# Performance work log

Measured on AMD Instinct MI355X. Metric: run time of the kernel, lower is better.

Reference implementation:

```python
import jax, jax.numpy as jnp
import numpy as np

HEADS = 4
DIM_HEAD = 128
DIM = 128
INNER = HEADS * DIM_HEAD  # 512
MAX_POS = 100
SCALE = DIM_HEAD ** -0.5


def setup_inputs() -> dict:
    key = jax.random.key(0)
    ks = jax.random.split(key, 8)
    b, h, w = 2, 48, 64
    fmap1 = jax.random.normal(ks[0], (b, DIM, h, w), jnp.float32)
    fmap2 = jax.random.normal(ks[1], (b, DIM, h, w), jnp.float32)
    Wqk = jax.random.normal(ks[2], (2 * INNER, DIM), jnp.float32) * 0.05
    Wv = jax.random.normal(ks[3], (INNER, DIM), jnp.float32) * 0.05
    rel_h = jax.random.normal(ks[4], (2 * MAX_POS - 1, DIM_HEAD), jnp.float32) * 0.05
    rel_w = jax.random.normal(ks[5], (2 * MAX_POS - 1, DIM_HEAD), jnp.float32) * 0.05
    Wp = jax.random.normal(ks[6], (DIM, INNER), jnp.float32) * 0.05
    gamma = jnp.full((1,), 0.1, jnp.float32)  # nonzero so the attn path is active
    return {"fmap1": fmap1, "fmap2": fmap2, "Wqk": Wqk, "Wv": Wv,
            "rel_h": rel_h, "rel_w": rel_w, "Wp": Wp, "gamma": gamma}


def _aggregate(fmap, Wqk, Wv, rel_h, rel_w, Wp, gamma):
    b, c, H, W = fmap.shape
    # 1x1 conv = channel matmul
    qk = jnp.einsum('oc,bchw->bohw', Wqk, fmap)
    q = qk[:, :INNER] * SCALE  # k chunk unused (position-only similarity)
    # b (n d) h w -> b n h w d
    q = q.reshape(b, HEADS, DIM_HEAD, H, W).transpose(0, 1, 3, 4, 2)
    v = jnp.einsum('oc,bchw->bohw', Wv, fmap)
    v = v.reshape(b, HEADS, DIM_HEAD, H, W).transpose(0, 1, 3, 4, 2).reshape(b, HEADS, H * W, DIM_HEAD)
    # relative position similarity (RelPosEmb)
    idx_h = jnp.arange(H)[:, None] - jnp.arange(H)[None, :] + (MAX_POS - 1)  # (H,H)
    idx_w = jnp.arange(W)[:, None] - jnp.arange(W)[None, :] + (MAX_POS - 1)  # (W,W)
    He = rel_h[idx_h]  # (x,u,d)
    We = rel_w[idx_w]  # (y,v,d)
    hs = jnp.einsum('bnxyd,xud->bnxyu', q, He)  # (b,n,x,y,u)
    ws = jnp.einsum('bnxyd,yvd->bnxyv', q, We)  # (b,n,x,y,v)
    sim = hs[..., :, None] + ws[..., None, :]   # (b,n,x,y,u,v)
    sim = sim.reshape(b, HEADS, H * W, H * W)
    attn = jax.nn.softmax(sim, axis=-1)
    out = jnp.einsum('bnij,bnjd->bnid', attn, v)  # (b,n,hw,d)
    out = out.reshape(b, HEADS, H, W, DIM_HEAD).transpose(0, 1, 4, 2, 3).reshape(b, INNER, H, W)
    out = jnp.einsum('oc,bchw->bohw', Wp, out)  # project (dim != inner_dim)
    return fmap + gamma[0] * out


def reference(fmap1, fmap2, Wqk, Wv, rel_h, rel_w, Wp, gamma):
    out1 = _aggregate(fmap1, Wqk, Wv, rel_h, rel_w, Wp, gamma)
    out2 = _aggregate(fmap2, Wqk, Wv, rel_h, rel_w, Wp, gamma)
    return (out1, out2)
```

## Files before the change

kernel.cpp:

```cpp
#include <hip/hip_runtime.h>
#include <cstdint>
#include <cstddef>

typedef short bf16x8 __attribute__((ext_vector_type(8)));
typedef float f32x4 __attribute__((ext_vector_type(4)));

#define HH 48
#define WW 64
#define HWSZ 3072
#define SCALE_Q 0.08838834764831845f

__device__ __forceinline__ float b2f(unsigned short u) {
    union { unsigned int i; float f; } c; c.i = ((unsigned int)u) << 16; return c.f;
}
__device__ __forceinline__ unsigned short f2b(float f) {
    union { float f; unsigned int i; } c; c.f = f;
    unsigned int r = (c.i + 0x7fffu + ((c.i >> 16) & 1u)) >> 16;
    return (unsigned short)r;
}

__global__ __launch_bounds__(256) void k_transpose(const float* __restrict__ f0,
                                                   const float* __restrict__ f1,
                                                   unsigned short* __restrict__ Xb) {
    __shared__ float t[32][33];
    int fb = blockIdx.z; int f = fb >> 1, bb = fb & 1;
    const float* src = f ? f1 : f0;
    int pT = blockIdx.x * 32, cT = blockIdx.y * 32;
    int tx = threadIdx.x, ty = threadIdx.y;
#pragma unroll
    for (int i = 0; i < 4; ++i) {
        int c = cT + ty + i * 8, pos = pT + tx;
        t[ty + i * 8][tx] = src[(size_t)(bb * 128 + c) * HWSZ + pos];
    }
    __syncthreads();
#pragma unroll
    for (int i = 0; i < 4; ++i) {
        int pos = pT + ty + i * 8, c = cT + tx;
        Xb[(size_t)(fb * HWSZ + pos) * 128 + c] = f2b(t[tx][ty + i * 8]);
    }
}

__global__ __launch_bounds__(256) void k_weights(const float* __restrict__ Wqk,
                                                 const float* __restrict__ Wv,
                                                 const float* __restrict__ Wp,
                                                 unsigned short* __restrict__ Wcat,
                                                 unsigned short* __restrict__ Wpb) {
    int idx = blockIdx.x * 256 + threadIdx.x;
    if (idx < 131072) {
        int o = idx >> 7, c = idx & 127;
        float v = (o < 512) ? Wqk[o * 128 + c] * SCALE_Q : Wv[(o - 512) * 128 + c];
        Wcat[idx] = f2b(v);
    } else {
        int j = idx - 131072;
        Wpb[j] = f2b(Wp[j]);
    }
}

__global__ __launch_bounds__(256) void k_qv(const unsigned short* __restrict__ Xb,
                                            const unsigned short* __restrict__ Wcat,
                                            unsigned short* __restrict__ Qx,
                                            unsigned short* __restrict__ Vt) {
    __shared__ unsigned short Asub[64 * 136];
    __shared__ unsigned short Bsub[128 * 136];
    int mt = blockIdx.x, nt = blockIdx.y, fb = blockIdx.z;
    int tid = threadIdx.x;
    const unsigned short* asrc = Xb + (size_t)(fb * HWSZ + mt * 64) * 128;
    const unsigned short* bsrc = Wcat + (size_t)nt * 128 * 128;
    for (int ch = tid; ch < 1024; ch += 256) {
        int row = ch >> 4, seg = ch & 15;
        *(bf16x8*)&Asub[row * 136 + seg * 8] = *(const bf16x8*)(asrc + ch * 8);
    }
    for (int ch = tid; ch < 2048; ch += 256) {
        int row = ch >> 4, seg = ch & 15;
        *(bf16x8*)&Bsub[row * 136 + seg * 8] = *(const bf16x8*)(bsrc + ch * 8);
    }
    __syncthreads();
    int l = tid & 63, w = tid >> 6;
    int wm = w >> 1, wn = w & 1;
    int lr = l & 15, lk8 = (l >> 4) * 8;
    f32x4 acc[2][4] = {};
#pragma unroll
    for (int kt = 0; kt < 4; ++kt) {
        bf16x8 a[2], b[4];
#pragma unroll
        for (int m = 0; m < 2; ++m)
            a[m] = *(const bf16x8*)&Asub[(wm * 32 + m * 16 + lr) * 136 + kt * 32 + lk8];
#pragma unroll
        for (int n = 0; n < 4; ++n)
            b[n] = *(const bf16x8*)&Bsub[(wn * 64 + n * 16 + lr) * 136 + kt * 32 + lk8];
#pragma unroll
        for (int m = 0; m < 2; ++m)
#pragma unroll
            for (int n = 0; n < 4; ++n)
                acc[m][n] = __builtin_amdgcn_mfma_f32_16x16x32_bf16(a[m], b[n], acc[m][n], 0, 0, 0);
    }
    int f = fb >> 1, bb = fb & 1;
#pragma unroll
    for (int m = 0; m < 2; ++m)
#pragma unroll
        for (int n = 0; n < 4; ++n) {
            int o = nt * 128 + wn * 64 + n * 16 + lr;
            int pos0 = mt * 64 + wm * 32 + m * 16 + (l >> 4) * 4;
            if (o < 512) {
                int nh = o >> 7, d = o & 127;
#pragma unroll
                for (int r = 0; r < 4; ++r) {
                    int pos = pos0 + r, x = pos >> 6, y = pos & 63;
                    Qx[(size_t)((f * 48 + x) * 512 + (bb * 4 + nh) * 64 + y) * 128 + d] = f2b(acc[m][n][r]);
                }
            } else {
                int oo = o - 512, nh = oo >> 7, d = oo & 127;
                uint2 val;
                val.x = (unsigned int)f2b(acc[m][n][0]) | ((unsigned int)f2b(acc[m][n][1]) << 16);
                val.y = (unsigned int)f2b(acc[m][n][2]) | ((unsigned int)f2b(acc[m][n][3]) << 16);
                *(uint2*)&Vt[(size_t)((fb * 4 + nh) * 128 + d) * HWSZ + pos0] = val;
            }
        }
}

__global__ __launch_bounds__(256) void k_ph(const unsigned short* __restrict__ Qx,
                                            const float* __restrict__ rel_h,
                                            unsigned short* __restrict__ PH) {
    __shared__ float sm[4][16][52];
    int x = blockIdx.x, f = blockIdx.y, mtz = blockIdx.z;
    int tid = threadIdx.x, l = tid & 63, w = tid >> 6;
    int lr = l & 15, lk8 = (l >> 4) * 8;
    bf16x8 bh[3][4];
#pragma unroll
    for (int ut = 0; ut < 3; ++ut) {
        int u = ut * 16 + lr, rr = x - u + 99;
#pragma unroll
        for (int kt = 0; kt < 4; ++kt) {
            const float* s = rel_h + rr * 128 + kt * 32 + lk8;
            float4 a0 = *(const float4*)s, a1 = *(const float4*)(s + 4);
            bf16x8 pk;
            pk[0] = (short)f2b(a0.x); pk[1] = (short)f2b(a0.y); pk[2] = (short)f2b(a0.z); pk[3] = (short)f2b(a0.w);
            pk[4] = (short)f2b(a1.x); pk[5] = (short)f2b(a1.y); pk[6] = (short)f2b(a1.z); pk[7] = (short)f2b(a1.w);
            bh[ut][kt] = pk;
        }
    }
    const unsigned short* qbase = Qx + (size_t)(f * 48 + x) * 512 * 128;
    unsigned short* phbase = PH + (size_t)(f * 48 + x) * 512 * 48;
    for (int mt = mtz * 2; mt < mtz * 2 + 2; ++mt) {
        int rg = w * 128 + mt * 16 + lr;
        const unsigned short* qrow = qbase + (size_t)rg * 128;
        bf16x8 a[4];
#pragma unroll
        for (int kt = 0; kt < 4; ++kt) a[kt] = *(const bf16x8*)(qrow + kt * 32 + lk8);
        f32x4 acc[3] = {};
#pragma unroll
        for (int kt = 0; kt < 4; ++kt)
#pragma unroll
            for (int ut = 0; ut < 3; ++ut)
                acc[ut] = __builtin_amdgcn_mfma_f32_16x16x32_bf16(a[kt], bh[ut][kt], acc[ut], 0, 0, 0);
        __syncthreads();
#pragma unroll
        for (int ut = 0; ut < 3; ++ut)
#pragma unroll
            for (int r = 0; r < 4; ++r)
                sm[w][(l >> 4) * 4 + r][ut * 16 + lr] = acc[ut][r];
        __syncthreads();
        int part = l >> 4;
        float vb[12];
        float mx = -1e30f;
#pragma unroll
        for (int j = 0; j < 12; ++j) { vb[j] = sm[w][lr][part * 12 + j]; mx = fmaxf(mx, vb[j]); }
        mx = fmaxf(mx, __shfl_xor(mx, 16, 64));
        mx = fmaxf(mx, __shfl_xor(mx, 32, 64));
        float ssum = 0.f;
#pragma unroll
        for (int j = 0; j < 12; ++j) { vb[j] = __expf(vb[j] - mx); ssum += vb[j]; }
        ssum += __shfl_xor(ssum, 16, 64);
        ssum += __shfl_xor(ssum, 32, 64);
        float inv = 1.0f / ssum;
        unsigned short* dst = phbase + (size_t)(w * 128 + mt * 16 + lr) * 48 + part * 12;
#pragma unroll
        for (int j = 0; j < 12; ++j) dst[j] = f2b(vb[j] * inv);
    }
}

__global__ __launch_bounds__(256) void k_pw(const unsigned short* __restrict__ Qx,
                                            const float* __restrict__ rel_w,
                                            unsigned short* __restrict__ PW) {
    __shared__ float sm[4][16][68];
    int y = blockIdx.x, f = blockIdx.y, mtz = blockIdx.z;
    int tid = threadIdx.x, l = tid & 63, w = tid >> 6;
    int lr = l & 15, lk8 = (l >> 4) * 8;
    bf16x8 bw[4][4];
#pragma unroll
    for (int vt = 0; vt < 4; ++vt) {
        int v = vt * 16 + lr, rr = y - v + 99;
#pragma unroll
        for (int kt = 0; kt < 4; ++kt) {
            const float* s = rel_w + rr * 128 + kt * 32 + lk8;
            float4 a0 = *(const float4*)s, a1 = *(const float4*)(s + 4);
            bf16x8 pk;
            pk[0] = (short)f2b(a0.x); pk[1] = (short)f2b(a0.y); pk[2] = (short)f2b(a0.z); pk[3] = (short)f2b(a0.w);
            pk[4] = (short)f2b(a1.x); pk[5] = (short)f2b(a1.y); pk[6] = (short)f2b(a1.z); pk[7] = (short)f2b(a1.w);
            bw[vt][kt] = pk;
        }
    }
    for (int mt = mtz * 2; mt < mtz * 2 + 2; ++mt) {
        int rg = w * 96 + mt * 16 + lr;
        int bn = rg / 48, xx = rg - bn * 48;
        const unsigned short* qrow = Qx + (size_t)((f * 48 + xx) * 512 + bn * 64 + y) * 128;
        bf16x8 a[4];
#pragma unroll
        for (int kt = 0; kt < 4; ++kt) a[kt] = *(const bf16x8*)(qrow + kt * 32 + lk8);
        f32x4 acc[4] = {};
#pragma unroll
        for (int kt = 0; kt < 4; ++kt)
#pragma unroll
            for (int vt = 0; vt < 4; ++vt)
                acc[vt] = __builtin_amdgcn_mfma_f32_16x16x32_bf16(a[kt], bw[vt][kt], acc[vt], 0, 0, 0);
        __syncthreads();
#pragma unroll
        for (int vt = 0; vt < 4; ++vt)
#pragma unroll
            for (int r = 0; r < 4; ++r)
                sm[w][(l >> 4) * 4 + r][vt * 16 + lr] = acc[vt][r];
        __syncthreads();
        int part = l >> 4;
        float vb[16];
        float mx = -1e30f;
#pragma unroll
        for (int j = 0; j < 16; ++j) { vb[j] = sm[w][lr][part * 16 + j]; mx = fmaxf(mx, vb[j]); }
        mx = fmaxf(mx, __shfl_xor(mx, 16, 64));
        mx = fmaxf(mx, __shfl_xor(mx, 32, 64));
        float ssum = 0.f;
#pragma unroll
        for (int j = 0; j < 16; ++j) { vb[j] = __expf(vb[j] - mx); ssum += vb[j]; }
        ssum += __shfl_xor(ssum, 16, 64);
        ssum += __shfl_xor(ssum, 32, 64);
        float inv = 1.0f / ssum;
        unsigned short* dst = PW + (size_t)((f * 64 + y) * 384 + rg) * 64 + part * 16;
#pragma unroll
        for (int j = 0; j < 16; ++j) dst[j] = f2b(vb[j] * inv);
    }
}

__global__ __launch_bounds__(256, 3) void k_attn(const unsigned short* __restrict__ PH,
                                                 const unsigned short* __restrict__ PW,
                                                 const unsigned short* __restrict__ Vt,
                                                 unsigned short* __restrict__ AO) {
    __shared__ unsigned short phl[48 * 128];
    __shared__ unsigned short vbuf[2][2][64 * 64];
    int bid = blockIdx.x;
    int r16 = bid & 15;
    int rest = bid >> 4;
    int t = rest >> 1, dh = rest & 1;
    int fbn = (r16 & 7) * 2 + (r16 >> 3);
    int f = fbn >> 3, bidx = (fbn >> 2) & 1, nh = fbn & 3;
    int fb = f * 2 + bidx, bn = bidx * 4 + nh;
    int tid = threadIdx.x;
    int l = tid & 63, wd = tid >> 6;
    int lr = l & 15, lg = l >> 4, lk8 = lg * 8;

    const unsigned short* vsrc = Vt + (size_t)((fb * 4 + nh) * 128 + dh * 64) * HWSZ;
    int sd = tid >> 3, sch = tid & 7;
    const unsigned short* vs0 = vsrc + (size_t)sd * HWSZ + sch * 8;
    const unsigned short* vs1 = vs0 + (size_t)32 * HWSZ;
    int wo0 = sd * 64 + ((sch ^ (sd & 7)) * 8);
    int wo1 = wo0 + 32 * 64;

    bf16x8 p0a = *(const bf16x8*)(vs0);
    bf16x8 p0b = *(const bf16x8*)(vs1);
    bf16x8 p1a = *(const bf16x8*)(vs0 + 64);
    bf16x8 p1b = *(const bf16x8*)(vs1 + 64);
    bf16x8 q0a = *(const bf16x8*)(vs0 + 128);
    bf16x8 q0b = *(const bf16x8*)(vs1 + 128);
    bf16x8 q1a = *(const bf16x8*)(vs0 + 192);
    bf16x8 q1b = *(const bf16x8*)(vs1 + 192);

    for (int i = tid; i < 3072; i += 256) {
        int up2 = i >> 7, q = i & 127;
        int xy = t * 128 + q, x = xy >> 6, y = xy & 63;
        unsigned int wv = *(const unsigned int*)(PH + ((size_t)(f * 48 + x) * 512 + bn * 64 + y) * 48 + up2 * 2);
        int qoff = (q & 15) * 8 + (q >> 4);
        phl[(up2 * 2) * 128 + qoff]     = (unsigned short)(wv & 0xffffu);
        phl[(up2 * 2 + 1) * 128 + qoff] = (unsigned short)(wv >> 16);
    }
    bf16x8 b[8][2];
#pragma unroll
    for (int n = 0; n < 8; ++n) {
        int xy = t * 128 + n * 16 + lr;
        int x = xy >> 6, y = xy & 63;
        const unsigned short* pwr = PW + ((size_t)(f * 64 + y) * 384 + bn * 48 + x) * 64;
        b[n][0] = *(const bf16x8*)(pwr + lk8);
        b[n][1] = *(const bf16x8*)(pwr + 32 + lk8);
    }
    *(bf16x8*)&vbuf[0][0][wo0] = p0a;
    *(bf16x8*)&vbuf[0][0][wo1] = p0b;
    *(bf16x8*)&vbuf[0][1][wo0] = p1a;
    *(bf16x8*)&vbuf[0][1][wo1] = p1b;
    __syncthreads();

    int arow = wd * 16 + lr;
    int ao0 = arow * 64 + ((lg ^ (arow & 7)) * 8);
    int ao1 = arow * 64 + (((4 + lg) ^ (arow & 7)) * 8);
    const unsigned short* phrow = &phl[lr * 8];
    f32x4 acc[8] = {};
    const f32x4 zero4 = {0.f, 0.f, 0.f, 0.f};
    for (int ph = 0; ph < 24; ++ph) {
        int cur = ph & 1;
        bf16x8 n0a = q0a, n0b = q0b, n1a = q1a, n1b = q1b;
        if (ph + 2 < 24) {
            const unsigned short* s0 = vs0 + (size_t)(2 * ph + 4) * 64;
            const unsigned short* s1 = vs1 + (size_t)(2 * ph + 4) * 64;
            n0a = *(const bf16x8*)(s0);
            n0b = *(const bf16x8*)(s1);
            n1a = *(const bf16x8*)(s0 + 64);
            n1b = *(const bf16x8*)(s1 + 64);
        }
        if (ph + 1 < 24) {
            *(bf16x8*)&vbuf[cur ^ 1][0][wo0] = q0a;
            *(bf16x8*)&vbuf[cur ^ 1][0][wo1] = q0b;
            *(bf16x8*)&vbuf[cur ^ 1][1][wo0] = q1a;
            *(bf16x8*)&vbuf[cur ^ 1][1][wo1] = q1b;
        }
#pragma unroll
        for (int uu = 0; uu < 2; ++uu) {
            int u = 2 * ph + uu;
            bf16x8 av0 = *(const bf16x8*)&vbuf[cur][uu][ao0];
            bf16x8 av1 = *(const bf16x8*)&vbuf[cur][uu][ao1];
            bf16x8 phv = *(const bf16x8*)(phrow + u * 128);
#pragma unroll
            for (int n = 0; n < 8; ++n) {
                f32x4 Y = __builtin_amdgcn_mfma_f32_16x16x32_bf16(av0, b[n][0], zero4, 0, 0, 0);
                Y = __builtin_amdgcn_mfma_f32_16x16x32_bf16(av1, b[n][1], Y, 0, 0, 0);
                float p = b2f((unsigned short)phv[n]);
                acc[n] += p * Y;
            }
        }
        __syncthreads();
        q0a = n0a; q0b = n0b; q1a = n1a; q1b = n1b;
    }
    unsigned short* aobase = AO + (size_t)fb * HWSZ * 512 + nh * 128 + dh * 64 + wd * 16 + lg * 4;
#pragma unroll
    for (int n = 0; n < 8; ++n) {
        int q = t * 128 + n * 16 + lr;
        uint2 val;
        val.x = (unsigned int)f2b(acc[n][0]) | ((unsigned int)f2b(acc[n][1]) << 16);
        val.y = (unsigned int)f2b(acc[n][2]) | ((unsigned int)f2b(acc[n][3]) << 16);
        *(uint2*)(aobase + (size_t)q * 512) = val;
    }
}

__global__ __launch_bounds__(256) void k_proj(const unsigned short* __restrict__ AO,
                                              const unsigned short* __restrict__ Wpb,
                                              const float* __restrict__ f0,
                                              const float* __restrict__ f1,
                                              const float* __restrict__ gamma,
                                              float* __restrict__ out) {
    __shared__ unsigned short Asub[64 * 136];
    __shared__ unsigned short Bsub[128 * 136];
    int t = blockIdx.x, fb = blockIdx.y;
    int f = fb >> 1, bb = fb & 1;
    int tid = threadIdx.x;
    int l = tid & 63, w = tid >> 6;
    int wm = w >> 1, wn = w & 1;
    int lr = l & 15, lk8 = (l >> 4) * 8;
    f32x4 acc[2][4] = {};
    for (int ks = 0; ks < 4; ++ks) {
        if (ks) __syncthreads();
        for (int ch = tid; ch < 1024; ch += 256) {
            int row = ch >> 4, seg = ch & 15;
            *(bf16x8*)&Asub[row * 136 + seg * 8] =
                *(const bf16x8*)(AO + (size_t)(fb * HWSZ + t * 64 + row) * 512 + ks * 128 + seg * 8);
        }
        for (int ch = tid; ch < 2048; ch += 256) {
            int row = ch >> 4, seg = ch & 15;
            *(bf16x8*)&Bsub[row * 136 + seg * 8] =
                *(const bf16x8*)(Wpb + (size_t)row * 512 + ks * 128 + seg * 8);
        }
        __syncthreads();
#pragma unroll
        for (int kt = 0; kt < 4; ++kt) {
            bf16x8 a[2], b[4];
#pragma unroll
            for (int m = 0; m < 2; ++m)
                a[m] = *(const bf16x8*)&Asub[(wm * 32 + m * 16 + lr) * 136 + kt * 32 + lk8];
#pragma unroll
            for (int n = 0; n < 4; ++n)
                b[n] = *(const bf16x8*)&Bsub[(wn * 64 + n * 16 + lr) * 136 + kt * 32 + lk8];
#pragma unroll
            for (int m = 0; m < 2; ++m)
#pragma unroll
                for (int n = 0; n < 4; ++n)
                    acc[m][n] = __builtin_amdgcn_mfma_f32_16x16x32_bf16(a[m], b[n], acc[m][n], 0, 0, 0);
        }
    }
    const float* fmapf = f ? f1 : f0;
    float g = gamma[0];
#pragma unroll
    for (int m = 0; m < 2; ++m)
#pragma unroll
        for (int n = 0; n < 4; ++n) {
            int c = wn * 64 + n * 16 + lr;
            int pos0 = t * 64 + wm * 32 + m * 16 + (l >> 4) * 4;
            size_t addr = (size_t)(bb * 128 + c) * HWSZ + pos0;
            float4 fv = *(const float4*)(fmapf + addr);
            float4 ov;
            ov.x = fv.x + g * acc[m][n][0];
            ov.y = fv.y + g * acc[m][n][1];
            ov.z = fv.z + g * acc[m][n][2];
            ov.w = fv.w + g * acc[m][n][3];
            *(float4*)(out + (size_t)f * 786432 + addr) = ov;
        }
}

extern "C" void kernel_launch(void* const* d_in, const int* in_sizes, int n_in,
                              void* d_out, int out_size, void* d_ws, size_t ws_size,
                              hipStream_t stream) {
    (void)in_sizes; (void)n_in; (void)out_size; (void)ws_size;
    const float* fmap1 = (const float*)d_in[0];
    const float* fmap2 = (const float*)d_in[1];
    const float* Wqk   = (const float*)d_in[2];
    const float* Wv    = (const float*)d_in[3];
    const float* rel_h = (const float*)d_in[4];
    const float* rel_w = (const float*)d_in[5];
    const float* Wp    = (const float*)d_in[6];
    const float* gamma = (const float*)d_in[7];
    float* out = (float*)d_out;
    char* ws = (char*)d_ws;

    unsigned short* Xb   = (unsigned short*)(ws + 0);
    unsigned short* Wcat = (unsigned short*)(ws + 3145728);
    unsigned short* Wpb  = (unsigned short*)(ws + 3407872);
    unsigned short* Qx   = (unsigned short*)(ws + 3538944);
    unsigned short* AO   = Qx;
    unsigned short* Vt   = (unsigned short*)(ws + 16121856);
    unsigned short* PH   = (unsigned short*)(ws + 28704768);
    unsigned short* PW   = (unsigned short*)(ws + 33423360);

    k_transpose<<<dim3(96, 4, 4), dim3(32, 8), 0, stream>>>(fmap1, fmap2, Xb);
    k_weights<<<dim3(768), dim3(256), 0, stream>>>(Wqk, Wv, Wp, Wcat, Wpb);
    k_qv<<<dim3(48, 8, 4), dim3(256), 0, stream>>>(Xb, Wcat, Qx, Vt);
    k_ph<<<dim3(48, 2, 4), dim3(256), 0, stream>>>(Qx, rel_h, PH);
    k_pw<<<dim3(64, 2, 3), dim3(256), 0, stream>>>(Qx, rel_w, PW);
    k_attn<<<dim3(768), dim3(256), 0, stream>>>(PH, PW, Vt, AO);
    k_proj<<<dim3(48, 4), dim3(256), 0, stream>>>(AO, Wpb, fmap1, fmap2, gamma, out);
}
```

Before: 116.6 us.

## Use direct global-to-LDS DMA for V tiles with per-row blocked V layout

V is now written by the projection kernel as a [fb,head,u,d,v] blocked layout, so each u-row's 128x64 tile is contiguous. The attention kernel then loads it with global_load_lds (16-byte DMA into LDS) and double-buffers it, replacing the register-staged prefetch followed by LDS stores. This removes the VGPR staging and the ds_write instructions, and it pre-swizzles global addresses so the LDS layout keeps the XOR bank pattern. The risk is that vmcnt(0) waits now stall on each phase's DMA, and correctness depends on the lane-to-LDS mapping of global_load_lds matching the swizzle.

```diff
diff --git a/kernel.cpp b/kernel.cpp
--- a/kernel.cpp
+++ b/kernel.cpp
@@ -17,6 +17,12 @@
     union { float f; unsigned int i; } c; c.f = f;
     unsigned int r = (c.i + 0x7fffu + ((c.i >> 16) & 1u)) >> 16;
     return (unsigned short)r;
+}
+
+__device__ __forceinline__ void dma16(const unsigned short* g, unsigned short* l) {
+    __builtin_amdgcn_global_load_lds((const __attribute__((address_space(1))) unsigned int*)g,
+                                     (__attribute__((address_space(3))) unsigned int*)l,
+                                     16, 0, 0);
 }
 
 __global__ __launch_bounds__(256) void k_transpose(const float* __restrict__ f0,
@@ -110,10 +116,11 @@
                 }
             } else {
                 int oo = o - 512, nh = oo >> 7, d = oo & 127;
+                int u = pos0 >> 6, v = pos0 & 63;
                 uint2 val;
                 val.x = (unsigned int)f2b(acc[m][n][0]) | ((unsigned int)f2b(acc[m][n][1]) << 16);
                 val.y = (unsigned int)f2b(acc[m][n][2]) | ((unsigned int)f2b(acc[m][n][3]) << 16);
-                *(uint2*)&Vt[(size_t)((fb * 4 + nh) * 128 + d) * HWSZ + pos0] = val;
+                *(uint2*)&Vt[(((size_t)(fb * 4 + nh) * 48 + u) * 128 + d) * 64 + v] = val;
             }
         }
 }
@@ -244,7 +251,7 @@
                                                  const unsigned short* __restrict__ Vt,
                                                  unsigned short* __restrict__ AO) {
     __shared__ unsigned short phl[48 * 128];
-    __shared__ unsigned short vbuf[2][2][64 * 64];
+    __shared__ unsigned short vbuf[2][2][4096];
     int bid = blockIdx.x;
     int r16 = bid & 15;
     int rest = bid >> 4;
@@ -256,21 +263,22 @@
     int l = tid & 63, wd = tid >> 6;
     int lr = l & 15, lg = l >> 4, lk8 = lg * 8;
 
-    const unsigned short* vsrc = Vt + (size_t)((fb * 4 + nh) * 128 + dh * 64) * HWSZ;
-    int sd = tid >> 3, sch = tid & 7;
-    const unsigned short* vs0 = vsrc + (size_t)sd * HWSZ + sch * 8;
-    const unsigned short* vs1 = vs0 + (size_t)32 * HWSZ;
-    int wo0 = sd * 64 + ((sch ^ (sd & 7)) * 8);
-    int wo1 = wo0 + 32 * 64;
-
-    bf16x8 p0a = *(const bf16x8*)(vs0);
-    bf16x8 p0b = *(const bf16x8*)(vs1);
-    bf16x8 p1a = *(const bf16x8*)(vs0 + 64);
-    bf16x8 p1b = *(const bf16x8*)(vs1 + 64);
-    bf16x8 q0a = *(const bf16x8*)(vs0 + 128);
-    bf16x8 q0b = *(const bf16x8*)(vs1 + 128);
-    bf16x8 q1a = *(const bf16x8*)(vs0 + 192);
-    bf16x8 q1b = *(const bf16x8*)(vs1 + 192);
+    const unsigned short* vhalf = Vt + (size_t)(fb * 4 + nh) * 48 * 8192 + dh * 4096;
+    int r0 = wd * 16 + (l >> 3), s0 = l & 7;
+    int r1 = r0 + 8;
+    int g0 = r0 * 64 + ((s0 ^ (r0 & 7)) * 8);
+    int g1 = r1 * 64 + ((s0 ^ (r1 & 7)) * 8);
+
+#define DMA_PHASE(BUF, U)                                                       \
+    {                                                                           \
+        const unsigned short* gt = vhalf + (size_t)(U) * 8192;                  \
+        dma16(gt + g0, &vbuf[BUF][0][wd * 1024]);                               \
+        dma16(gt + g1, &vbuf[BUF][0][wd * 1024 + 512]);                         \
+        dma16(gt + 8192 + g0, &vbuf[BUF][1][wd * 1024]);                        \
+        dma16(gt + 8192 + g1, &vbuf[BUF][1][wd * 1024 + 512]);                  \
+    }
+
+    DMA_PHASE(0, 0);
 
     for (int i = tid; i < 3072; i += 256) {
         int up2 = i >> 7, q = i & 127;
@@ -289,10 +297,7 @@
         b[n][0] = *(const bf16x8*)(pwr + lk8);
         b[n][1] = *(const bf16x8*)(pwr + 32 + lk8);
     }
-    *(bf16x8*)&vbuf[0][0][wo0] = p0a;
-    *(bf16x8*)&vbuf[0][0][wo1] = p0b;
-    *(bf16x8*)&vbuf[0][1][wo0] = p1a;
-    *(bf16x8*)&vbuf[0][1][wo1] = p1b;
+    asm volatile("s_waitcnt vmcnt(0)" ::: "memory");
     __syncthreads();
 
     int arow = wd * 16 + lr;
@@ -301,26 +306,13 @@
     const unsigned short* phrow = &phl[lr * 8];
     f32x4 acc[8] = {};
     const f32x4 zero4 = {0.f, 0.f, 0.f, 0.f};
-    for (int ph = 0; ph < 24; ++ph) {
-        int cur = ph & 1;
-        bf16x8 n0a = q0a, n0b = q0b, n1a = q1a, n1b = q1b;
-        if (ph + 2 < 24) {
-            const unsigned short* s0 = vs0 + (size_t)(2 * ph + 4) * 64;
-            const unsigned short* s1 = vs1 + (size_t)(2 * ph + 4) * 64;
-            n0a = *(const bf16x8*)(s0);
-            n0b = *(const bf16x8*)(s1);
-            n1a = *(const bf16x8*)(s0 + 64);
-            n1b = *(const bf16x8*)(s1 + 64);
-        }
-        if (ph + 1 < 24) {
-            *(bf16x8*)&vbuf[cur ^ 1][0][wo0] = q0a;
-            *(bf16x8*)&vbuf[cur ^ 1][0][wo1] = q0b;
-            *(bf16x8*)&vbuf[cur ^ 1][1][wo0] = q1a;
-            *(bf16x8*)&vbuf[cur ^ 1][1][wo1] = q1b;
-        }
+
+    for (int p = 0; p < 24; ++p) {
+        int cur = p & 1;
+        if (p + 1 < 24) DMA_PHASE(cur ^ 1, 2 * (p + 1));
 #pragma unroll
         for (int uu = 0; uu < 2; ++uu) {
-            int u = 2 * ph + uu;
+            int u = 2 * p + uu;
             bf16x8 av0 = *(const bf16x8*)&vbuf[cur][uu][ao0];
             bf16x8 av1 = *(const bf16x8*)&vbuf[cur][uu][ao1];
             bf16x8 phv = *(const bf16x8*)(phrow + u * 128);
@@ -328,13 +320,14 @@
             for (int n = 0; n < 8; ++n) {
                 f32x4 Y = __builtin_amdgcn_mfma_f32_16x16x32_bf16(av0, b[n][0], zero4, 0, 0, 0);
                 Y = __builtin_amdgcn_mfma_f32_16x16x32_bf16(av1, b[n][1], Y, 0, 0, 0);
-                float p = b2f((unsigned short)phv[n]);
-                acc[n] += p * Y;
+                acc[n] += b2f((unsigned short)phv[n]) * Y;
             }
         }
-        __syncthreads();
-        q0a = n0a; q0b = n0b; q1a = n1a; q1b = n1b;
-    }
+        asm volatile("s_waitcnt vmcnt(0)" ::: "memory");
+        __syncthreads();
+    }
+#undef DMA_PHASE
+
     unsigned short* aobase = AO + (size_t)fb * HWSZ * 512 + nh * 128 + dh * 64 + wd * 16 + lg * 4;
 #pragma unroll
     for (int n = 0; n < 8; ++n) {
```

Measured after the change: 116.5 us. No clear change (-0.0%).
